# Kernel tuning notes

Measured on AMD Instinct MI355X. Metric: run time of the kernel, lower is better.

## Reference

```python
import jax, jax.numpy as jnp
import numpy as np

K_TOKENS = 40  # safety_token_count
LN_EPS = 1e-5


def setup_inputs() -> dict:
    key = jax.random.key(0)
    ks = jax.random.split(key, 3)
    B, S, D = 16, 4096, 768
    H = D // 2
    features = jax.random.normal(ks[0], (B, S, D), dtype=jnp.float32)
    W1 = jax.random.normal(ks[1], (D, H), dtype=jnp.float32) * (1.0 / np.sqrt(D))
    b1 = jnp.zeros((H,), dtype=jnp.float32)
    ln_gamma = jnp.ones((H,), dtype=jnp.float32)
    ln_beta = jnp.zeros((H,), dtype=jnp.float32)
    W2 = jax.random.normal(ks[2], (H, 1), dtype=jnp.float32) * (1.0 / np.sqrt(H))
    b2 = jnp.zeros((1,), dtype=jnp.float32)
    return {"features": features, "W1": W1, "b1": b1,
            "ln_gamma": ln_gamma, "ln_beta": ln_beta, "W2": W2, "b2": b2}


def _scores(features, W1, b1, ln_gamma, ln_beta, W2, b2):
    # Linear -> LayerNorm -> GELU(exact) -> Dropout(eval=identity) -> Linear -> Sigmoid
    h = jnp.einsum('bsd,dh->bsh', features, W1) + b1
    mu = jnp.mean(h, axis=-1, keepdims=True)
    var = jnp.mean(jnp.square(h - mu), axis=-1, keepdims=True)
    h = (h - mu) * jax.lax.rsqrt(var + LN_EPS) * ln_gamma + ln_beta
    h = jax.nn.gelu(h, approximate=False)
    s = jnp.einsum('bsh,ho->bso', h, W2) + b2  # [B, S, 1]
    return jax.nn.sigmoid(s[..., 0])           # [B, S]


def reference(features, W1, b1, ln_gamma, ln_beta, W2, b2):
    scores = _scores(features, W1, b1, ln_gamma, ln_beta, W2, b2)
    k = min(K_TOKENS, features.shape[1])
    _, indices = jax.lax.top_k(scores, k)                      # [B, k]
    safety_tokens = jnp.take_along_axis(features, indices[:, :, None], axis=1)  # [B, k, D]
    return safety_tokens, indices
```

## Files before the change

kernel.cpp:

```cpp
#include <hip/hip_runtime.h>
#include <hip/hip_bf16.h>
#include <math.h>

#define B_   16
#define S_   4096
#define D_   768
#define H_   384
#define NTOK (B_ * S_)
#define KTOP 40
#define NTILES 24
#define KCH    24

typedef __attribute__((ext_vector_type(8))) short bf16x8;
typedef __attribute__((ext_vector_type(4))) float f32x4;

static __device__ __forceinline__ unsigned short f2bf(float x) {
    __hip_bfloat16 h = __float2bfloat16(x);
    unsigned short r;
    __builtin_memcpy(&r, &h, sizeof(r));
    return r;
}
static __device__ __forceinline__ float bf2f(unsigned short h) {
    union { unsigned u; float f; } v; v.u = ((unsigned)h) << 16; return v.f;
}

#define KBARRIER()                                                \
    do {                                                          \
        asm volatile("s_waitcnt lgkmcnt(0)" ::: "memory");        \
        __builtin_amdgcn_s_barrier();                             \
        asm volatile("" ::: "memory");                            \
    } while (0)

__global__ __launch_bounds__(64) void pack_w1(const float* __restrict__ W1,
                                              unsigned short* __restrict__ bh,
                                              unsigned short* __restrict__ bl)
{
    const int nt   = blockIdx.x;
    const int ch   = blockIdx.y;
    const int lane = threadIdx.x;
    const int n    = nt * 16 + (lane & 15);
    const int k0   = ch * 32 + (lane >> 4) * 8;

    unsigned short h8[8], l8[8];
#pragma unroll
    for (int j = 0; j < 8; ++j) {
        const float v = W1[(size_t)(k0 + j) * H_ + n];
        const unsigned short h = f2bf(v);
        h8[j] = h;
        l8[j] = f2bf(v - bf2f(h));
    }
    const size_t base = ((size_t)(nt * KCH + ch) * 64 + lane) * 8;
#pragma unroll
    for (int j = 0; j < 8; ++j) { bh[base + j] = h8[j]; bl[base + j] = l8[j]; }
}

__global__ __launch_bounds__(256, 4) void score_kernel(
    const float* __restrict__ features,
    const unsigned short* __restrict__ bh_g,
    const unsigned short* __restrict__ bl_g,
    const float* __restrict__ b1,
    const float* __restrict__ gamma,
    const float* __restrict__ beta,
    const float* __restrict__ W2,
    const float* __restrict__ b2,
    float* __restrict__ scores)
{
    __shared__ unsigned short Ah[32][40];
    __shared__ unsigned short Al[32][40];
    __shared__ float red[4][32];
    __shared__ float mu_s[32];
    __shared__ float rs_s[32];

    const int tid  = threadIdx.x;
    const int lane = tid & 63;
    const int w    = tid >> 6;
    const int base = blockIdx.x * 32;
    const int cl   = lane & 15;
    const int p    = lane >> 4;

    f32x4 acc[2][6];
#pragma unroll
    for (int m = 0; m < 2; ++m)
#pragma unroll
        for (int t = 0; t < 6; ++t) acc[m][t] = (f32x4){0.f, 0.f, 0.f, 0.f};

    const int r0 = tid >> 3, c0 = (tid & 7) * 4;
    const float* arow = features + (size_t)(base + r0) * D_ + c0;

    float4 p0 = *(const float4*)(arow);

    for (int c = 0; c < KCH; ++c) {
        if (c) KBARRIER();
        {
            unsigned short h0 = f2bf(p0.x), h1 = f2bf(p0.y), h2 = f2bf(p0.z), h3 = f2bf(p0.w);
            Ah[r0][c0] = h0; Ah[r0][c0+1] = h1; Ah[r0][c0+2] = h2; Ah[r0][c0+3] = h3;
            Al[r0][c0]   = f2bf(p0.x - bf2f(h0));
            Al[r0][c0+1] = f2bf(p0.y - bf2f(h1));
            Al[r0][c0+2] = f2bf(p0.z - bf2f(h2));
            Al[r0][c0+3] = f2bf(p0.w - bf2f(h3));
        }
        KBARRIER();

        if (c + 1 < KCH) {
            p0 = *(const float4*)(arow + (c + 1) * 32);
        }

        bf16x8 ahf[2], alf[2];
#pragma unroll
        for (int m = 0; m < 2; ++m) {
            const int row = m * 16 + cl;
            ahf[m] = *(const bf16x8*)&Ah[row][p * 8];
            alf[m] = *(const bf16x8*)&Al[row][p * 8];
        }
#pragma unroll
        for (int t = 0; t < 6; ++t) {
            const size_t bb = ((size_t)((w * 6 + t) * KCH + c) * 64 + lane) * 8;
            const bf16x8 bhf = *(const bf16x8*)(bh_g + bb);
            const bf16x8 blf = *(const bf16x8*)(bl_g + bb);
#pragma unroll
            for (int m = 0; m < 2; ++m) {
                acc[m][t] = __builtin_amdgcn_mfma_f32_16x16x32_bf16(ahf[m], bhf, acc[m][t], 0, 0, 0);
                acc[m][t] = __builtin_amdgcn_mfma_f32_16x16x32_bf16(ahf[m], blf, acc[m][t], 0, 0, 0);
                acc[m][t] = __builtin_amdgcn_mfma_f32_16x16x32_bf16(alf[m], bhf, acc[m][t], 0, 0, 0);
            }
        }
    }

    float b1v[6], gv[6], bev[6], w2v[6];
#pragma unroll
    for (int t = 0; t < 6; ++t) {
        const int n = (w * 6 + t) * 16 + cl;
        b1v[t] = b1[n]; gv[t] = gamma[n]; bev[t] = beta[n]; w2v[t] = W2[n];
    }
#pragma unroll
    for (int m = 0; m < 2; ++m)
#pragma unroll
        for (int t = 0; t < 6; ++t)
#pragma unroll
            for (int r = 0; r < 4; ++r) acc[m][t][r] += b1v[t];

#pragma unroll
    for (int m = 0; m < 2; ++m) {
        float sm[4] = {0.f, 0.f, 0.f, 0.f};
#pragma unroll
        for (int t = 0; t < 6; ++t)
#pragma unroll
            for (int r = 0; r < 4; ++r) sm[r] += acc[m][t][r];
#pragma unroll
        for (int r = 0; r < 4; ++r) {
#pragma unroll
            for (int off = 1; off <= 8; off <<= 1) sm[r] += __shfl_xor(sm[r], off, 64);
        }
        if (cl == 0) {
#pragma unroll
            for (int r = 0; r < 4; ++r) red[w][m * 16 + p * 4 + r] = sm[r];
        }
    }
    __syncthreads();
    if (tid < 32) mu_s[tid] = (red[0][tid] + red[1][tid] + red[2][tid] + red[3][tid]) * (1.0f / H_);
    __syncthreads();

#pragma unroll
    for (int m = 0; m < 2; ++m) {
        float mur[4];
#pragma unroll
        for (int r = 0; r < 4; ++r) mur[r] = mu_s[m * 16 + p * 4 + r];
        float sm[4] = {0.f, 0.f, 0.f, 0.f};
#pragma unroll
        for (int t = 0; t < 6; ++t)
#pragma unroll
            for (int r = 0; r < 4; ++r) { const float d = acc[m][t][r] - mur[r]; sm[r] += d * d; }
#pragma unroll
        for (int r = 0; r < 4; ++r) {
#pragma unroll
            for (int off = 1; off <= 8; off <<= 1) sm[r] += __shfl_xor(sm[r], off, 64);
        }
        if (cl == 0) {
#pragma unroll
            for (int r = 0; r < 4; ++r) red[w][m * 16 + p * 4 + r] = sm[r];
        }
    }
    __syncthreads();
    if (tid < 32) rs_s[tid] = rsqrtf((red[0][tid] + red[1][tid] + red[2][tid] + red[3][tid]) * (1.0f / H_) + 1e-5f);
    __syncthreads();

#pragma unroll
    for (int m = 0; m < 2; ++m) {
        float mur[4], rsr[4];
#pragma unroll
        for (int r = 0; r < 4; ++r) { mur[r] = mu_s[m * 16 + p * 4 + r]; rsr[r] = rs_s[m * 16 + p * 4 + r]; }
        float sm[4] = {0.f, 0.f, 0.f, 0.f};
#pragma unroll
        for (int t = 0; t < 6; ++t)
#pragma unroll
            for (int r = 0; r < 4; ++r) {
                const float y  = (acc[m][t][r] - mur[r]) * rsr[r] * gv[t] + bev[t];
                const float ge = 0.5f * y * (1.0f + erff(y * 0.70710678118654752f));
                sm[r] = fmaf(ge, w2v[t], sm[r]);
            }
#pragma unroll
        for (int r = 0; r < 4; ++r) {
#pragma unroll
            for (int off = 1; off <= 8; off <<= 1) sm[r] += __shfl_xor(sm[r], off, 64);
        }
        if (cl == 0) {
#pragma unroll
            for (int r = 0; r < 4; ++r) red[w][m * 16 + p * 4 + r] = sm[r];
        }
    }
    __syncthreads();
    if (tid < 32) {
        const float s = red[0][tid] + red[1][tid] + red[2][tid] + red[3][tid] + b2[0];
        scores[base + tid] = 1.0f / (1.0f + expf(-s));
    }
}

__global__ __launch_bounds__(256) void select_kernel(const float* __restrict__ scores,
                                                     int* __restrict__ sel)
{
    __shared__ unsigned int bits_s[S_];
    __shared__ unsigned int hist[256];
    __shared__ unsigned int suf[256];
    __shared__ unsigned int wtot[4];
    __shared__ int s_byte, s_rem;
    __shared__ unsigned int s_ngt, s_neq;
    __shared__ unsigned int candV[64];
    __shared__ int candI[64];
    __shared__ int eqI[256];

    const int b    = blockIdx.x;
    const int tid  = threadIdx.x;
    const int lane = tid & 63;
    const int w4   = tid >> 6;

    for (int i = tid; i < S_; i += 256)
        bits_s[i] = __float_as_uint(scores[b * S_ + i]);
    if (tid == 0) { s_rem = KTOP; s_ngt = 0u; s_neq = 0u; }

    unsigned int prefix = 0u, mask = 0u;
    for (int pb = 3; pb >= 0; --pb) {
        hist[tid] = 0u;
        __syncthreads();
        for (int i = tid; i < S_; i += 256) {
            const unsigned int u = bits_s[i];
            if ((u & mask) == prefix) atomicAdd(&hist[(u >> (8 * pb)) & 255u], 1u);
        }
        __syncthreads();
        {
            unsigned int v = hist[tid];
#pragma unroll
            for (int off = 1; off < 64; off <<= 1) {
                const unsigned int y = __shfl_down(v, off, 64);
                if (lane + off < 64) v += y;
            }
            if (lane == 0) wtot[w4] = v;
            __syncthreads();
            unsigned int add = 0u;
#pragma unroll
            for (int j = 0; j < 4; ++j) if (j > w4) add += wtot[j];
            v += add;
            suf[tid] = v;
            __syncthreads();
            const int rem = s_rem;
            const unsigned int nxt = (tid < 255) ? suf[tid + 1] : 0u;
            if (suf[tid] >= (unsigned)rem && (tid == 255 || nxt < (unsigned)rem)) {
                s_byte = tid;
                s_rem  = rem - (int)nxt;
            }
        }
        __syncthreads();
        prefix |= ((unsigned int)s_byte) << (8 * pb);
        mask   |= 0xFFu << (8 * pb);
        __syncthreads();
    }
    const unsigned int T = prefix;
    const int need = s_rem;

    for (int i = tid; i < S_; i += 256) {
        const unsigned int u = bits_s[i];
        if (u > T) {
            const unsigned int pos = atomicAdd(&s_ngt, 1u);
            candV[pos] = u; candI[pos] = i;
        } else if (u == T) {
            const unsigned int pos = atomicAdd(&s_neq, 1u);
            if (pos < 256u) eqI[pos] = i;
        }
    }
    __syncthreads();
    const int ngt = (int)s_ngt;
    const int neq = (int)(s_neq < 256u ? s_neq : 256u);
    for (int j = tid; j < neq; j += 256) {
        int rank = 0;
        for (int l = 0; l < neq; ++l) rank += (eqI[l] < eqI[j]) ? 1 : 0;
        if (rank < need) { candV[ngt + rank] = T; candI[ngt + rank] = eqI[j]; }
    }
    __syncthreads();
    if (tid < KTOP) {
        const unsigned int u = candV[tid];
        const int idx = candI[tid];
        int rank = 0;
        for (int j = 0; j < KTOP; ++j)
            rank += (candV[j] > u || (candV[j] == u && candI[j] < idx)) ? 1 : 0;
        sel[b * KTOP + rank] = idx;
    }
}

__global__ __launch_bounds__(192) void gather_kernel(const float* __restrict__ features,
                                                     const int* __restrict__ sel,
                                                     float* __restrict__ out_tok,
                                                     float* __restrict__ out_idx)
{
    const int i = blockIdx.x;
    const int b = blockIdx.y;
    const int idx = sel[b * KTOP + i];
    const float4* src = (const float4*)(features + ((size_t)b * S_ + idx) * D_);
    float4* dst = (float4*)(out_tok + ((size_t)b * KTOP + i) * D_);
    dst[threadIdx.x] = src[threadIdx.x];
    if (threadIdx.x == 0) out_idx[b * KTOP + i] = (float)idx;
}

extern "C" void kernel_launch(void* const* d_in, const int* in_sizes, int n_in,
                              void* d_out, int out_size, void* d_ws, size_t ws_size,
                              hipStream_t stream)
{
    const float* features = (const float*)d_in[0];
    const float* W1       = (const float*)d_in[1];
    const float* b1       = (const float*)d_in[2];
    const float* gamma    = (const float*)d_in[3];
    const float* beta     = (const float*)d_in[4];
    const float* W2       = (const float*)d_in[5];
    const float* b2       = (const float*)d_in[6];

    unsigned short* bh = (unsigned short*)d_ws;
    unsigned short* bl = bh + (size_t)D_ * H_;
    float* scores      = (float*)(bl + (size_t)D_ * H_);
    int*   sel         = (int*)(scores + NTOK);

    float* out        = (float*)d_out;
    float* out_tokens = out;
    float* out_idx    = out + (size_t)B_ * KTOP * D_;

    pack_w1<<<dim3(NTILES, KCH), 64, 0, stream>>>(W1, bh, bl);
    score_kernel<<<NTOK / 32, 256, 0, stream>>>(features, bh, bl, b1, gamma, beta, W2, b2, scores);
    select_kernel<<<B_, 256, 0, stream>>>(scores, sel);
    gather_kernel<<<dim3(KTOP, B_), 192, 0, stream>>>(features, sel, out_tokens, out_idx);
}
```

Measured before the change: 429.5 us.

## Score all tokens in single bf16, rescore top-128 candidates in fp32

Replaces the 3-pass split-bf16 MFMA scoring (hi/lo for both operands) with a single bf16 MFMA pass. This cuts matrix work by about two thirds and drops the lo-part loads and LDS traffic. To keep the selection accurate, a radix-select now picks 128 candidates per batch, rescores them in full fp32, and does a final rank to choose the top 40. The cost is extra small kernels, and candidates near the cutoff could be misordered if bf16 error pushes a true top-40 token below rank 128.

After: 511.4 us. 1.19x slower.

```diff
diff --git a/kernel.cpp b/kernel.cpp
--- a/kernel.cpp
+++ b/kernel.cpp
@@ -8,6 +8,7 @@
 #define H_   384
 #define NTOK (B_ * S_)
 #define KTOP 40
+#define NCAND 128
 #define NTILES 24
 #define KCH    24
 
@@ -19,9 +20,6 @@
     unsigned short r;
     __builtin_memcpy(&r, &h, sizeof(r));
     return r;
-}
-static __device__ __forceinline__ float bf2f(unsigned short h) {
-    union { unsigned u; float f; } v; v.u = ((unsigned)h) << 16; return v.f;
 }
 
 #define KBARRIER()                                                \
@@ -32,8 +30,7 @@
     } while (0)
 
 __global__ __launch_bounds__(64) void pack_w1(const float* __restrict__ W1,
-                                              unsigned short* __restrict__ bh,
-                                              unsigned short* __restrict__ bl)
+                                              unsigned short* __restrict__ bh)
 {
     const int nt   = blockIdx.x;
     const int ch   = blockIdx.y;
@@ -41,23 +38,18 @@
     const int n    = nt * 16 + (lane & 15);
     const int k0   = ch * 32 + (lane >> 4) * 8;
 
-    unsigned short h8[8], l8[8];
-#pragma unroll
-    for (int j = 0; j < 8; ++j) {
-        const float v = W1[(size_t)(k0 + j) * H_ + n];
-        const unsigned short h = f2bf(v);
-        h8[j] = h;
-        l8[j] = f2bf(v - bf2f(h));
-    }
+    unsigned short h8[8];
+#pragma unroll
+    for (int j = 0; j < 8; ++j)
+        h8[j] = f2bf(W1[(size_t)(k0 + j) * H_ + n]);
     const size_t base = ((size_t)(nt * KCH + ch) * 64 + lane) * 8;
 #pragma unroll
-    for (int j = 0; j < 8; ++j) { bh[base + j] = h8[j]; bl[base + j] = l8[j]; }
-}
-
-__global__ __launch_bounds__(256, 4) void score_kernel(
+    for (int j = 0; j < 8; ++j) bh[base + j] = h8[j];
+}
+
+__global__ __launch_bounds__(256, 5) void score_kernel(
     const float* __restrict__ features,
     const unsigned short* __restrict__ bh_g,
-    const unsigned short* __restrict__ bl_g,
     const float* __restrict__ b1,
     const float* __restrict__ gamma,
     const float* __restrict__ beta,
@@ -66,7 +58,6 @@
     float* __restrict__ scores)
 {
     __shared__ unsigned short Ah[32][40];
-    __shared__ unsigned short Al[32][40];
     __shared__ float red[4][32];
     __shared__ float mu_s[32];
     __shared__ float rs_s[32];
@@ -91,38 +82,25 @@
 
     for (int c = 0; c < KCH; ++c) {
         if (c) KBARRIER();
-        {
-            unsigned short h0 = f2bf(p0.x), h1 = f2bf(p0.y), h2 = f2bf(p0.z), h3 = f2bf(p0.w);
-            Ah[r0][c0] = h0; Ah[r0][c0+1] = h1; Ah[r0][c0+2] = h2; Ah[r0][c0+3] = h3;
-            Al[r0][c0]   = f2bf(p0.x - bf2f(h0));
-            Al[r0][c0+1] = f2bf(p0.y - bf2f(h1));
-            Al[r0][c0+2] = f2bf(p0.z - bf2f(h2));
-            Al[r0][c0+3] = f2bf(p0.w - bf2f(h3));
-        }
+        Ah[r0][c0]   = f2bf(p0.x);
+        Ah[r0][c0+1] = f2bf(p0.y);
+        Ah[r0][c0+2] = f2bf(p0.z);
+        Ah[r0][c0+3] = f2bf(p0.w);
         KBARRIER();
 
-        if (c + 1 < KCH) {
-            p0 = *(const float4*)(arow + (c + 1) * 32);
-        }
-
-        bf16x8 ahf[2], alf[2];
-#pragma unroll
-        for (int m = 0; m < 2; ++m) {
-            const int row = m * 16 + cl;
-            ahf[m] = *(const bf16x8*)&Ah[row][p * 8];
-            alf[m] = *(const bf16x8*)&Al[row][p * 8];
-        }
+        if (c + 1 < KCH) p0 = *(const float4*)(arow + (c + 1) * 32);
+
+        bf16x8 ahf[2];
+#pragma unroll
+        for (int m = 0; m < 2; ++m)
+            ahf[m] = *(const bf16x8*)&Ah[m * 16 + cl][p * 8];
 #pragma unroll
         for (int t = 0; t < 6; ++t) {
             const size_t bb = ((size_t)((w * 6 + t) * KCH + c) * 64 + lane) * 8;
             const bf16x8 bhf = *(const bf16x8*)(bh_g + bb);
-            const bf16x8 blf = *(const bf16x8*)(bl_g + bb);
-#pragma unroll
-            for (int m = 0; m < 2; ++m) {
+#pragma unroll
+            for (int m = 0; m < 2; ++m)
                 acc[m][t] = __builtin_amdgcn_mfma_f32_16x16x32_bf16(ahf[m], bhf, acc[m][t], 0, 0, 0);
-                acc[m][t] = __builtin_amdgcn_mfma_f32_16x16x32_bf16(ahf[m], blf, acc[m][t], 0, 0, 0);
-                acc[m][t] = __builtin_amdgcn_mfma_f32_16x16x32_bf16(alf[m], bhf, acc[m][t], 0, 0, 0);
-            }
         }
     }
 
@@ -215,8 +193,8 @@
     }
 }
 
-__global__ __launch_bounds__(256) void select_kernel(const float* __restrict__ scores,
-                                                     int* __restrict__ sel)
+__global__ __launch_bounds__(256) void cand_kernel(const float* __restrict__ scores,
+                                                   int* __restrict__ cand)
 {
     __shared__ unsigned int bits_s[S_];
     __shared__ unsigned int hist[256];
@@ -224,8 +202,8 @@
     __shared__ unsigned int wtot[4];
     __shared__ int s_byte, s_rem;
     __shared__ unsigned int s_ngt, s_neq;
-    __shared__ unsigned int candV[64];
-    __shared__ int candI[64];
+    __shared__ unsigned int candV[NCAND];
+    __shared__ int candI[NCAND];
     __shared__ int eqI[256];
 
     const int b    = blockIdx.x;
@@ -235,7 +213,7 @@
 
     for (int i = tid; i < S_; i += 256)
         bits_s[i] = __float_as_uint(scores[b * S_ + i]);
-    if (tid == 0) { s_rem = KTOP; s_ngt = 0u; s_neq = 0u; }
+    if (tid == 0) { s_rem = NCAND; s_ngt = 0u; s_neq = 0u; }
 
     unsigned int prefix = 0u, mask = 0u;
     for (int pb = 3; pb >= 0; --pb) {
@@ -295,14 +273,109 @@
         if (rank < need) { candV[ngt + rank] = T; candI[ngt + rank] = eqI[j]; }
     }
     __syncthreads();
-    if (tid < KTOP) {
-        const unsigned int u = candV[tid];
-        const int idx = candI[tid];
-        int rank = 0;
-        for (int j = 0; j < KTOP; ++j)
-            rank += (candV[j] > u || (candV[j] == u && candI[j] < idx)) ? 1 : 0;
-        sel[b * KTOP + rank] = idx;
-    }
+    if (tid < NCAND) cand[b * NCAND + tid] = candI[tid];
+}
+
+__global__ __launch_bounds__(256) void rescore_kernel(
+    const float* __restrict__ features,
+    const float* __restrict__ W1,
+    const float* __restrict__ b1,
+    const float* __restrict__ gamma,
+    const float* __restrict__ beta,
+    const float* __restrict__ W2,
+    const float* __restrict__ b2,
+    const int* __restrict__ cand,
+    float* __restrict__ escore)
+{
+    __shared__ float xs[8][D_];
+    __shared__ int cidx[8];
+
+    const int g   = blockIdx.x;
+    const int b   = blockIdx.y;
+    const int tid = threadIdx.x;
+
+    if (tid < 8) cidx[tid] = cand[b * NCAND + g * 8 + tid];
+    __syncthreads();
+
+    for (int i = tid; i < 8 * (D_ / 4); i += 256) {
+        const int r = i / (D_ / 4);
+        const int c = i % (D_ / 4);
+        *(float4*)&xs[r][c * 4] =
+            *(const float4*)(features + ((size_t)b * S_ + cidx[r]) * D_ + c * 4);
+    }
+    __syncthreads();
+
+    const int r  = tid >> 5;
+    const int ln = tid & 31;
+    const int n0 = ln * 12;
+
+    float h[12];
+#pragma unroll
+    for (int j = 0; j < 12; ++j) h[j] = b1[n0 + j];
+
+    for (int d = 0; d < D_; ++d) {
+        const float xv = xs[r][d];
+        const float4 w0 = *(const float4*)(W1 + (size_t)d * H_ + n0);
+        const float4 w1 = *(const float4*)(W1 + (size_t)d * H_ + n0 + 4);
+        const float4 w2 = *(const float4*)(W1 + (size_t)d * H_ + n0 + 8);
+        h[0] = fmaf(xv, w0.x, h[0]);  h[1] = fmaf(xv, w0.y, h[1]);
+        h[2] = fmaf(xv, w0.z, h[2]);  h[3] = fmaf(xv, w0.w, h[3]);
+        h[4] = fmaf(xv, w1.x, h[4]);  h[5] = fmaf(xv, w1.y, h[5]);
+        h[6] = fmaf(xv, w1.z, h[6]);  h[7] = fmaf(xv, w1.w, h[7]);
+        h[8] = fmaf(xv, w2.x, h[8]);  h[9] = fmaf(xv, w2.y, h[9]);
+        h[10] = fmaf(xv, w2.z, h[10]); h[11] = fmaf(xv, w2.w, h[11]);
+    }
+
+    float sm = 0.f;
+#pragma unroll
+    for (int j = 0; j < 12; ++j) sm += h[j];
+#pragma unroll
+    for (int off = 1; off < 32; off <<= 1) sm += __shfl_xor(sm, off, 32);
+    const float mu = sm * (1.0f / H_);
+
+    float sv = 0.f;
+#pragma unroll
+    for (int j = 0; j < 12; ++j) { const float d = h[j] - mu; sv += d * d; }
+#pragma unroll
+    for (int off = 1; off < 32; off <<= 1) sv += __shfl_xor(sv, off, 32);
+    const float rsig = rsqrtf(sv * (1.0f / H_) + 1e-5f);
+
+    float ss = 0.f;
+#pragma unroll
+    for (int j = 0; j < 12; ++j) {
+        const int n = n0 + j;
+        const float y  = (h[j] - mu) * rsig * gamma[n] + beta[n];
+        const float ge = 0.5f * y * (1.0f + erff(y * 0.70710678118654752f));
+        ss = fmaf(ge, W2[n], ss);
+    }
+#pragma unroll
+    for (int off = 1; off < 32; off <<= 1) ss += __shfl_xor(ss, off, 32);
+
+    if (ln == 0) {
+        const float s = ss + b2[0];
+        escore[b * NCAND + g * 8 + r] = 1.0f / (1.0f + expf(-s));
+    }
+}
+
+__global__ __launch_bounds__(NCAND) void final_kernel(const float* __restrict__ escore,
+                                                      const int* __restrict__ cand,
+                                                      int* __restrict__ sel)
+{
+    __shared__ float s_s[NCAND];
+    __shared__ int   s_i[NCAND];
+    const int b   = blockIdx.x;
+    const int tid = threadIdx.x;
+
+    s_s[tid] = escore[b * NCAND + tid];
+    s_i[tid] = cand[b * NCAND + tid];
+    __syncthreads();
+
+    const float s = s_s[tid];
+    const int   idx = s_i[tid];
+    int rank = 0;
+    for (int l = 0; l < NCAND; ++l)
+        rank += (s_s[l] > s || (s_s[l] == s && s_i[l] < idx)) ? 1 : 0;
+    if (rank < KTOP) sel[b * KTOP + rank] = idx;
 }
 
 __global__ __launch_bounds__(192) void gather_kernel(const float* __restrict__ features,
@@ -332,16 +405,20 @@
     const float* b2       = (const float*)d_in[6];
 
     unsigned short* bh = (unsigned short*)d_ws;
-    unsigned short* bl = bh + (size_t)D_ * H_;
-    float* scores      = (float*)(bl + (size_t)D_ * H_);
-    int*   sel         = (int*)(scores + NTOK);
+    float* scores      = (float*)(bh + (size_t)D_ * H_);
+    int*   cand        = (int*)(scores + NTOK);
+    float* escore      = (float*)(cand + B_ * NCAND);
+    int*   sel         = (int*)(escore + B_ * NCAND);
 
     float* out        = (float*)d_out;
     float* out_tokens = out;
     float* out_idx    = out + (size_t)B_ * KTOP * D_;
 
-    pack_w1<<<dim3(NTILES, KCH), 64, 0, stream>>>(W1, bh, bl);
-    score_kernel<<<NTOK / 32, 256, 0, stream>>>(features, bh, bl, b1, gamma, beta, W2, b2, scores);
-    select_kernel<<<B_, 256, 0, stream>>>(scores, sel);
+    pack_w1<<<dim3(NTILES, KCH), 64, 0, stream>>>(W1, bh);
+    score_kernel<<<NTOK / 32, 256, 0, stream>>>(features, bh, b1, gamma, beta, W2, b2, scores);
+    cand_kernel<<<B_, 256, 0, stream>>>(scores, cand);
+    rescore_kernel<<<dim3(B_ * NCAND / (8 * 16), B_), 256, 0, stream>>>(
+        features, W1, b1, gamma, beta, W2, b2, cand, escore);
+    final_kernel<<<B_, NCAND, 0, stream>>>(escore, cand, sel);
     gather_kernel<<<dim3(KTOP, B_), 192, 0, stream>>>(features, sel, out_tokens, out_idx);
 }
```

## Score all tokens in single bf16, rescore top-128 candidates in split precision

Applied to the files above, without the earlier changes.

The full-token score pass now uses one bf16 MFMA per tile instead of three split-precision products. Each wave computes its 16 rows across all 384 hidden columns, so the shared-memory staging, block barriers and cross-wave LayerNorm reductions go away. A candidate pass keeps the top 128 tokens per batch by coarse score, and these are rescored with the original three-term bf16 hi/lo method before the final top-40 ranking. The main risk is that single-bf16 error could push a true top-40 token outside the 128 candidates.

New measurement: 643.9 us. 49.9% more time.

```diff
diff --git a/kernel.cpp b/kernel.cpp
--- a/kernel.cpp
+++ b/kernel.cpp
@@ -8,6 +8,7 @@
 #define H_   384
 #define NTOK (B_ * S_)
 #define KTOP 40
+#define NCAND 128
 #define NTILES 24
 #define KCH    24
 
@@ -41,23 +42,19 @@
     const int n    = nt * 16 + (lane & 15);
     const int k0   = ch * 32 + (lane >> 4) * 8;
 
-    unsigned short h8[8], l8[8];
+    const size_t dst = ((size_t)(ch * NTILES + nt) * 64 + lane) * 8;
 #pragma unroll
     for (int j = 0; j < 8; ++j) {
         const float v = W1[(size_t)(k0 + j) * H_ + n];
         const unsigned short h = f2bf(v);
-        h8[j] = h;
-        l8[j] = f2bf(v - bf2f(h));
-    }
-    const size_t base = ((size_t)(nt * KCH + ch) * 64 + lane) * 8;
-#pragma unroll
-    for (int j = 0; j < 8; ++j) { bh[base + j] = h8[j]; bl[base + j] = l8[j]; }
-}
-
-__global__ __launch_bounds__(256, 4) void score_kernel(
+        bh[dst + j] = h;
+        bl[dst + j] = f2bf(v - bf2f(h));
+    }
+}
+
+__global__ __launch_bounds__(256, 3) void score_kernel(
     const float* __restrict__ features,
     const unsigned short* __restrict__ bh_g,
-    const unsigned short* __restrict__ bl_g,
     const float* __restrict__ b1,
     const float* __restrict__ gamma,
     const float* __restrict__ beta,
@@ -65,158 +62,105 @@
     const float* __restrict__ b2,
     float* __restrict__ scores)
 {
-    __shared__ unsigned short Ah[32][40];
-    __shared__ unsigned short Al[32][40];
-    __shared__ float red[4][32];
-    __shared__ float mu_s[32];
-    __shared__ float rs_s[32];
-
     const int tid  = threadIdx.x;
     const int lane = tid & 63;
     const int w    = tid >> 6;
-    const int base = blockIdx.x * 32;
     const int cl   = lane & 15;
     const int p    = lane >> 4;
-
-    f32x4 acc[2][6];
-#pragma unroll
-    for (int m = 0; m < 2; ++m)
-#pragma unroll
-        for (int t = 0; t < 6; ++t) acc[m][t] = (f32x4){0.f, 0.f, 0.f, 0.f};
-
-    const int r0 = tid >> 3, c0 = (tid & 7) * 4;
-    const float* arow = features + (size_t)(base + r0) * D_ + c0;
-
-    float4 p0 = *(const float4*)(arow);
+    const int rowbase = blockIdx.x * 64 + w * 16;
+
+    f32x4 acc[24];
+#pragma unroll
+    for (int t = 0; t < 24; ++t) acc[t] = (f32x4){0.f, 0.f, 0.f, 0.f};
+
+    const float* arow = features + (size_t)(rowbase + cl) * D_ + p * 8;
+
+    float4 a0 = *(const float4*)(arow);
+    float4 a1 = *(const float4*)(arow + 4);
 
     for (int c = 0; c < KCH; ++c) {
-        if (c) KBARRIER();
-        {
-            unsigned short h0 = f2bf(p0.x), h1 = f2bf(p0.y), h2 = f2bf(p0.z), h3 = f2bf(p0.w);
-            Ah[r0][c0] = h0; Ah[r0][c0+1] = h1; Ah[r0][c0+2] = h2; Ah[r0][c0+3] = h3;
-            Al[r0][c0]   = f2bf(p0.x - bf2f(h0));
-            Al[r0][c0+1] = f2bf(p0.y - bf2f(h1));
-            Al[r0][c0+2] = f2bf(p0.z - bf2f(h2));
-            Al[r0][c0+3] = f2bf(p0.w - bf2f(h3));
-        }
-        KBARRIER();
-
+        float4 n0, n1;
         if (c + 1 < KCH) {
-            p0 = *(const float4*)(arow + (c + 1) * 32);
-        }
-
-        bf16x8 ahf[2], alf[2];
-#pragma unroll
-        for (int m = 0; m < 2; ++m) {
-            const int row = m * 16 + cl;
-            ahf[m] = *(const bf16x8*)&Ah[row][p * 8];
-            alf[m] = *(const bf16x8*)&Al[row][p * 8];
-        }
-#pragma unroll
-        for (int t = 0; t < 6; ++t) {
-            const size_t bb = ((size_t)((w * 6 + t) * KCH + c) * 64 + lane) * 8;
-            const bf16x8 bhf = *(const bf16x8*)(bh_g + bb);
-            const bf16x8 blf = *(const bf16x8*)(bl_g + bb);
-#pragma unroll
-            for (int m = 0; m < 2; ++m) {
-                acc[m][t] = __builtin_amdgcn_mfma_f32_16x16x32_bf16(ahf[m], bhf, acc[m][t], 0, 0, 0);
-                acc[m][t] = __builtin_amdgcn_mfma_f32_16x16x32_bf16(ahf[m], blf, acc[m][t], 0, 0, 0);
-                acc[m][t] = __builtin_amdgcn_mfma_f32_16x16x32_bf16(alf[m], bhf, acc[m][t], 0, 0, 0);
+            n0 = *(const float4*)(arow + (c + 1) * 32);
+            n1 = *(const float4*)(arow + (c + 1) * 32 + 4);
+        }
+        bf16x8 ah;
+        ah[0] = (short)f2bf(a0.x); ah[1] = (short)f2bf(a0.y);
+        ah[2] = (short)f2bf(a0.z); ah[3] = (short)f2bf(a0.w);
+        ah[4] = (short)f2bf(a1.x); ah[5] = (short)f2bf(a1.y);
+        ah[6] = (short)f2bf(a1.z); ah[7] = (short)f2bf(a1.w);
+
+        const unsigned short* bb = bh_g + (size_t)c * (NTILES * 64 * 8) + lane * 8;
+#pragma unroll
+        for (int t = 0; t < 24; ++t) {
+            const bf16x8 bf = *(const bf16x8*)(bb + t * (64 * 8));
+            acc[t] = __builtin_amdgcn_mfma_f32_16x16x32_bf16(ah, bf, acc[t], 0, 0, 0);
+        }
+        if (c + 1 < KCH) { a0 = n0; a1 = n1; }
+    }
+
+#pragma unroll
+    for (int t = 0; t < 24; ++t) {
+        const float bv = b1[t * 16 + cl];
+#pragma unroll
+        for (int r = 0; r < 4; ++r) acc[t][r] += bv;
+    }
+    float mu[4];
+    {
+        float sm[4] = {0.f, 0.f, 0.f, 0.f};
+#pragma unroll
+        for (int t = 0; t < 24; ++t)
+#pragma unroll
+            for (int r = 0; r < 4; ++r) sm[r] += acc[t][r];
+#pragma unroll
+        for (int r = 0; r < 4; ++r) {
+#pragma unroll
+            for (int off = 1; off <= 8; off <<= 1) sm[r] += __shfl_xor(sm[r], off, 64);
+            mu[r] = sm[r] * (1.0f / H_);
+        }
+    }
+    float rs[4];
+    {
+        float sv[4] = {0.f, 0.f, 0.f, 0.f};
+#pragma unroll
+        for (int t = 0; t < 24; ++t)
+#pragma unroll
+            for (int r = 0; r < 4; ++r) { const float d = acc[t][r] - mu[r]; sv[r] += d * d; }
+#pragma unroll
+        for (int r = 0; r < 4; ++r) {
+#pragma unroll
+            for (int off = 1; off <= 8; off <<= 1) sv[r] += __shfl_xor(sv[r], off, 64);
+            rs[r] = rsqrtf(sv[r] * (1.0f / H_) + 1e-5f);
+        }
+    }
+    {
+        float ss[4] = {0.f, 0.f, 0.f, 0.f};
+#pragma unroll
+        for (int t = 0; t < 24; ++t) {
+            const int n = t * 16 + cl;
+            const float gv = gamma[n], bev = beta[n], wv = W2[n];
+#pragma unroll
+            for (int r = 0; r < 4; ++r) {
+                const float y  = (acc[t][r] - mu[r]) * rs[r] * gv + bev;
+                const float ge = 0.5f * y * (1.0f + erff(y * 0.70710678118654752f));
+                ss[r] = fmaf(ge, wv, ss[r]);
             }
         }
-    }
-
-    float b1v[6], gv[6], bev[6], w2v[6];
-#pragma unroll
-    for (int t = 0; t < 6; ++t) {
-        const int n = (w * 6 + t) * 16 + cl;
-        b1v[t] = b1[n]; gv[t] = gamma[n]; bev[t] = beta[n]; w2v[t] = W2[n];
-    }
-#pragma unroll
-    for (int m = 0; m < 2; ++m)
-#pragma unroll
-        for (int t = 0; t < 6; ++t)
-#pragma unroll
-            for (int r = 0; r < 4; ++r) acc[m][t][r] += b1v[t];
-
-#pragma unroll
-    for (int m = 0; m < 2; ++m) {
-        float sm[4] = {0.f, 0.f, 0.f, 0.f};
-#pragma unroll
-        for (int t = 0; t < 6; ++t)
-#pragma unroll
-            for (int r = 0; r < 4; ++r) sm[r] += acc[m][t][r];
-#pragma unroll
-        for (int r = 0; r < 4; ++r) {
-#pragma unroll
-            for (int off = 1; off <= 8; off <<= 1) sm[r] += __shfl_xor(sm[r], off, 64);
+#pragma unroll
+        for (int r = 0; r < 4; ++r) {
+#pragma unroll
+            for (int off = 1; off <= 8; off <<= 1) ss[r] += __shfl_xor(ss[r], off, 64);
         }
         if (cl == 0) {
 #pragma unroll
-            for (int r = 0; r < 4; ++r) red[w][m * 16 + p * 4 + r] = sm[r];
-        }
-    }
-    __syncthreads();
-    if (tid < 32) mu_s[tid] = (red[0][tid] + red[1][tid] + red[2][tid] + red[3][tid]) * (1.0f / H_);
-    __syncthreads();
-
-#pragma unroll
-    for (int m = 0; m < 2; ++m) {
-        float mur[4];
-#pragma unroll
-        for (int r = 0; r < 4; ++r) mur[r] = mu_s[m * 16 + p * 4 + r];
-        float sm[4] = {0.f, 0.f, 0.f, 0.f};
-#pragma unroll
-        for (int t = 0; t < 6; ++t)
-#pragma unroll
-            for (int r = 0; r < 4; ++r) { const float d = acc[m][t][r] - mur[r]; sm[r] += d * d; }
-#pragma unroll
-        for (int r = 0; r < 4; ++r) {
-#pragma unroll
-            for (int off = 1; off <= 8; off <<= 1) sm[r] += __shfl_xor(sm[r], off, 64);
-        }
-        if (cl == 0) {
-#pragma unroll
-            for (int r = 0; r < 4; ++r) red[w][m * 16 + p * 4 + r] = sm[r];
-        }
-    }
-    __syncthreads();
-    if (tid < 32) rs_s[tid] = rsqrtf((red[0][tid] + red[1][tid] + red[2][tid] + red[3][tid]) * (1.0f / H_) + 1e-5f);
-    __syncthreads();
-
-#pragma unroll
-    for (int m = 0; m < 2; ++m) {
-        float mur[4], rsr[4];
-#pragma unroll
-        for (int r = 0; r < 4; ++r) { mur[r] = mu_s[m * 16 + p * 4 + r]; rsr[r] = rs_s[m * 16 + p * 4 + r]; }
-        float sm[4] = {0.f, 0.f, 0.f, 0.f};
-#pragma unroll
-        for (int t = 0; t < 6; ++t)
-#pragma unroll
-            for (int r = 0; r < 4; ++r) {
-                const float y  = (acc[m][t][r] - mur[r]) * rsr[r] * gv[t] + bev[t];
-                const float ge = 0.5f * y * (1.0f + erff(y * 0.70710678118654752f));
-                sm[r] = fmaf(ge, w2v[t], sm[r]);
-            }
-#pragma unroll
-        for (int r = 0; r < 4; ++r) {
-#pragma unroll
-            for (int off = 1; off <= 8; off <<= 1) sm[r] += __shfl_xor(sm[r], off, 64);
-        }
-        if (cl == 0) {
-#pragma unroll
-            for (int r = 0; r < 4; ++r) red[w][m * 16 + p * 4 + r] = sm[r];
-        }
-    }
-    __syncthreads();
-    if (tid < 32) {
-        const float s = red[0][tid] + red[1][tid] + red[2][tid] + red[3][tid] + b2[0];
-        scores[base + tid] = 1.0f / (1.0f + expf(-s));
-    }
-}
-
-__global__ __launch_bounds__(256) void select_kernel(const float* __restrict__ scores,
-                                                     int* __restrict__ sel)
+            for (int r = 0; r < 4; ++r)
+                scores[rowbase + p * 4 + r] = 1.0f / (1.0f + expf(-(ss[r] + b2[0])));
+        }
+    }
+}
+
+__global__ __launch_bounds__(256) void cand_kernel(const float* __restrict__ scores,
+                                                   int* __restrict__ cand)
 {
     __shared__ unsigned int bits_s[S_];
     __shared__ unsigned int hist[256];
@@ -224,8 +168,8 @@
     __shared__ unsigned int wtot[4];
     __shared__ int s_byte, s_rem;
     __shared__ unsigned int s_ngt, s_neq;
-    __shared__ unsigned int candV[64];
-    __shared__ int candI[64];
+    __shared__ unsigned int candV[NCAND];
+    __shared__ int candI[NCAND];
     __shared__ int eqI[256];
 
     const int b    = blockIdx.x;
@@ -235,7 +179,7 @@
 
     for (int i = tid; i < S_; i += 256)
         bits_s[i] = __float_as_uint(scores[b * S_ + i]);
-    if (tid == 0) { s_rem = KTOP; s_ngt = 0u; s_neq = 0u; }
+    if (tid == 0) { s_rem = NCAND; s_ngt = 0u; s_neq = 0u; }
 
     unsigned int prefix = 0u, mask = 0u;
     for (int pb = 3; pb >= 0; --pb) {
@@ -295,14 +239,190 @@
         if (rank < need) { candV[ngt + rank] = T; candI[ngt + rank] = eqI[j]; }
     }
     __syncthreads();
-    if (tid < KTOP) {
-        const unsigned int u = candV[tid];
-        const int idx = candI[tid];
-        int rank = 0;
-        for (int j = 0; j < KTOP; ++j)
-            rank += (candV[j] > u || (candV[j] == u && candI[j] < idx)) ? 1 : 0;
-        sel[b * KTOP + rank] = idx;
-    }
+    if (tid < NCAND) cand[b * NCAND + tid] = candI[tid];
+}
+
+__global__ __launch_bounds__(256, 4) void rescore_kernel(
+    const float* __restrict__ features,
+    const unsigned short* __restrict__ bh_g,
+    const unsigned short* __restrict__ bl_g,
+    const float* __restrict__ b1,
+    const float* __restrict__ gamma,
+    const float* __restrict__ beta,
+    const float* __restrict__ W2,
+    const float* __restrict__ b2,
+    const int* __restrict__ cand,
+    float* __restrict__ escore)
+{
+    __shared__ unsigned short Ah[32][40];
+    __shared__ unsigned short Al[32][40];
+    __shared__ float red[4][32];
+    __shared__ float mu_s[32];
+    __shared__ float rs_s[32];
+
+    const int tid  = threadIdx.x;
+    const int lane = tid & 63;
+    const int w    = tid >> 6;
+    const int g    = blockIdx.x;
+    const int b    = blockIdx.y;
+    const int cl   = lane & 15;
+    const int p    = lane >> 4;
+
+    f32x4 acc[2][6];
+#pragma unroll
+    for (int m = 0; m < 2; ++m)
+#pragma unroll
+        for (int t = 0; t < 6; ++t) acc[m][t] = (f32x4){0.f, 0.f, 0.f, 0.f};
+
+    const int r0 = tid >> 3, c0 = (tid & 7) * 4;
+    const int ci = cand[b * NCAND + g * 32 + r0];
+    const float* arow = features + ((size_t)b * S_ + ci) * D_ + c0;
+
+    float4 p0 = *(const float4*)(arow);
+
+    for (int c = 0; c < KCH; ++c) {
+        if (c) KBARRIER();
+        {
+            unsigned short h0 = f2bf(p0.x), h1 = f2bf(p0.y), h2 = f2bf(p0.z), h3 = f2bf(p0.w);
+            Ah[r0][c0] = h0; Ah[r0][c0+1] = h1; Ah[r0][c0+2] = h2; Ah[r0][c0+3] = h3;
+            Al[r0][c0]   = f2bf(p0.x - bf2f(h0));
+            Al[r0][c0+1] = f2bf(p0.y - bf2f(h1));
+            Al[r0][c0+2] = f2bf(p0.z - bf2f(h2));
+            Al[r0][c0+3] = f2bf(p0.w - bf2f(h3));
+        }
+        KBARRIER();
+
+        if (c + 1 < KCH) p0 = *(const float4*)(arow + (c + 1) * 32);
+
+        bf16x8 ahf[2], alf[2];
+#pragma unroll
+        for (int m = 0; m < 2; ++m) {
+            const int row = m * 16 + cl;
+            ahf[m] = *(const bf16x8*)&Ah[row][p * 8];
+            alf[m] = *(const bf16x8*)&Al[row][p * 8];
+        }
+#pragma unroll
+        for (int t = 0; t < 6; ++t) {
+            const size_t bb = ((size_t)(c * NTILES + (w * 6 + t)) * 64 + lane) * 8;
+            const bf16x8 bhf = *(const bf16x8*)(bh_g + bb);
+            const bf16x8 blf = *(const bf16x8*)(bl_g + bb);
+#pragma unroll
+            for (int m = 0; m < 2; ++m) {
+                acc[m][t] = __builtin_amdgcn_mfma_f32_16x16x32_bf16(ahf[m], bhf, acc[m][t], 0, 0, 0);
+                acc[m][t] = __builtin_amdgcn_mfma_f32_16x16x32_bf16(ahf[m], blf, acc[m][t], 0, 0, 0);
+                acc[m][t] = __builtin_amdgcn_mfma_f32_16x16x32_bf16(alf[m], bhf, acc[m][t], 0, 0, 0);
+            }
+        }
+    }
+
+    float b1v[6], gv[6], bev[6], w2v[6];
+#pragma unroll
+    for (int t = 0; t < 6; ++t) {
+        const int n = (w * 6 + t) * 16 + cl;
+        b1v[t] = b1[n]; gv[t] = gamma[n]; bev[t] = beta[n]; w2v[t] = W2[n];
+    }
+#pragma unroll
+    for (int m = 0; m < 2; ++m)
+#pragma unroll
+        for (int t = 0; t < 6; ++t)
+#pragma unroll
+            for (int r = 0; r < 4; ++r) acc[m][t][r] += b1v[t];
+
+#pragma unroll
+    for (int m = 0; m < 2; ++m) {
+        float sm[4] = {0.f, 0.f, 0.f, 0.f};
+#pragma unroll
+        for (int t = 0; t < 6; ++t)
+#pragma unroll
+            for (int r = 0; r < 4; ++r) sm[r] += acc[m][t][r];
+#pragma unroll
+        for (int r = 0; r < 4; ++r) {
+#pragma unroll
+            for (int off = 1; off <= 8; off <<= 1) sm[r] += __shfl_xor(sm[r], off, 64);
+        }
+        if (cl == 0) {
+#pragma unroll
+            for (int r = 0; r < 4; ++r) red[w][m * 16 + p * 4 + r] = sm[r];
+        }
+    }
+    __syncthreads();
+    if (tid < 32) mu_s[tid] = (red[0][tid] + red[1][tid] + red[2][tid] + red[3][tid]) * (1.0f / H_);
+    __syncthreads();
+
+#pragma unroll
+    for (int m = 0; m < 2; ++m) {
+        float mur[4];
+#pragma unroll
+        for (int r = 0; r < 4; ++r) mur[r] = mu_s[m * 16 + p * 4 + r];
+        float sm[4] = {0.f, 0.f, 0.f, 0.f};
+#pragma unroll
+        for (int t = 0; t < 6; ++t)
+#pragma unroll
+            for (int r = 0; r < 4; ++r) { const float d = acc[m][t][r] - mur[r]; sm[r] += d * d; }
+#pragma unroll
+        for (int r = 0; r < 4; ++r) {
+#pragma unroll
+            for (int off = 1; off <= 8; off <<= 1) sm[r] += __shfl_xor(sm[r], off, 64);
+        }
+        if (cl == 0) {
+#pragma unroll
+            for (int r = 0; r < 4; ++r) red[w][m * 16 + p * 4 + r] = sm[r];
+        }
+    }
+    __syncthreads();
+    if (tid < 32) rs_s[tid] = rsqrtf((red[0][tid] + red[1][tid] + red[2][tid] + red[3][tid]) * (1.0f / H_) + 1e-5f);
+    __syncthreads();
+
+#pragma unroll
+    for (int m = 0; m < 2; ++m) {
+        float mur[4], rsr[4];
+#pragma unroll
+        for (int r = 0; r < 4; ++r) { mur[r] = mu_s[m * 16 + p * 4 + r]; rsr[r] = rs_s[m * 16 + p * 4 + r]; }
+        float sm[4] = {0.f, 0.f, 0.f, 0.f};
+#pragma unroll
+        for (int t = 0; t < 6; ++t)
+#pragma unroll
+            for (int r = 0; r < 4; ++r) {
+                const float y  = (acc[m][t][r] - mur[r]) * rsr[r] * gv[t] + bev[t];
+                const float ge = 0.5f * y * (1.0f + erff(y * 0.70710678118654752f));
+                sm[r] = fmaf(ge, w2v[t], sm[r]);
+            }
+#pragma unroll
+        for (int r = 0; r < 4; ++r) {
+#pragma unroll
+            for (int off = 1; off <= 8; off <<= 1) sm[r] += __shfl_xor(sm[r], off, 64);
+        }
+        if (cl == 0) {
+#pragma unroll
+            for (int r = 0; r < 4; ++r) red[w][m * 16 + p * 4 + r] = sm[r];
+        }
+    }
+    __syncthreads();
+    if (tid < 32) {
+        const float s = red[0][tid] + red[1][tid] + red[2][tid] + red[3][tid] + b2[0];
+        escore[b * NCAND + g * 32 + tid] = 1.0f / (1.0f + expf(-s));
+    }
+}
+
+__global__ __launch_bounds__(NCAND) void final_kernel(const float* __restrict__ escore,
+                                                      const int* __restrict__ cand,
+                                                      int* __restrict__ sel)
+{
+    __shared__ float s_s[NCAND];
+    __shared__ int   s_i[NCAND];
+    const int b   = blockIdx.x;
+    const int tid = threadIdx.x;
+
+    s_s[tid] = escore[b * NCAND + tid];
+    s_i[tid] = cand[b * NCAND + tid];
+    __syncthreads();
+
+    const float s = s_s[tid];
+    const int   idx = s_i[tid];
+    int rank = 0;
+    for (int l = 0; l < NCAND; ++l)
+        rank += (s_s[l] > s || (s_s[l] == s && s_i[l] < idx)) ? 1 : 0;
+    if (rank < KTOP) sel[b * KTOP + rank] = idx;
 }
 
 __global__ __launch_bounds__(192) void gather_kernel(const float* __restrict__ features,
@@ -334,14 +454,19 @@
     unsigned short* bh = (unsigned short*)d_ws;
     unsigned short* bl = bh + (size_t)D_ * H_;
     float* scores      = (float*)(bl + (size_t)D_ * H_);
-    int*   sel         = (int*)(scores + NTOK);
+    int*   cand        = (int*)(scores + NTOK);
+    float* escore      = (float*)(cand + B_ * NCAND);
+    int*   sel         = (int*)(escore + B_ * NCAND);
 
     float* out        = (float*)d_out;
     float* out_tokens = out;
     float* out_idx    = out + (size_t)B_ * KTOP * D_;
 
     pack_w1<<<dim3(NTILES, KCH), 64, 0, stream>>>(W1, bh, bl);
-    score_kernel<<<NTOK / 32, 256, 0, stream>>>(features, bh, bl, b1, gamma, beta, W2, b2, scores);
-    select_kernel<<<B_, 256, 0, stream>>>(scores, sel);
+    score_kernel<<<NTOK / 64, 256, 0, stream>>>(features, bh, b1, gamma, beta, W2, b2, scores);
+    cand_kernel<<<B_, 256, 0, stream>>>(scores, cand);
+    rescore_kernel<<<dim3(NCAND / 32, B_), 256, 0, stream>>>(
+        features, bh, bl, b1, gamma, beta, W2, b2, cand, escore);
+    final_kernel<<<B_, NCAND, 0, stream>>>(escore, cand, sel);
     gather_kernel<<<dim3(KTOP, B_), 192, 0, stream>>>(features, sel, out_tokens, out_idx);
 }
```
